# Kernel tuning notes

Hardware: AMD Instinct MI355X
Metric: run time of the kernel (lower is better)

## Reference

```python
import jax, jax.numpy as jnp
import numpy as np

NUM_EMBEDDINGS = 8192
EMBEDDING_DIM = 512
COMMITMENT_COST = 0.25


def setup_inputs() -> dict:
    key = jax.random.key(0)
    k1, k2 = jax.random.split(key)
    x = jax.random.normal(k1, (32768, EMBEDDING_DIM), dtype=jnp.float32)
    embeddings = jax.random.normal(k2, (NUM_EMBEDDINGS, EMBEDDING_DIM), dtype=jnp.float32) * 0.1
    return {"x": x, "embeddings": embeddings}


def reference(x, embeddings):
    # Flatten to (N, D)
    orig_shape = x.shape
    flat_x = x.reshape(-1, EMBEDDING_DIM)
    n = flat_x.shape[0]

    x_sq = jnp.sum(flat_x * flat_x, axis=1, keepdims=True)
    e_sq = jnp.sum(embeddings * embeddings, axis=1)
    dist = x_sq + e_sq - 2.0 * jnp.matmul(flat_x, embeddings.T)
    encoding_indices = jnp.argmin(dist, axis=1)  # (N,)

    # Codebook lookup (equivalent to one_hot @ embeddings)
    quantized = embeddings[encoding_indices].reshape(orig_shape)

    # Straight-through estimator
    quantized_st = x + jax.lax.stop_gradient(quantized - x)

    # Commitment loss (quantized detached)
    commitment_loss = COMMITMENT_COST * jnp.mean(
        (x - jax.lax.stop_gradient(quantized)) ** 2
    )

    # Perplexity from mean one-hot encodings (= normalized counts)
    counts = jnp.zeros((NUM_EMBEDDINGS,), dtype=jnp.float32).at[encoding_indices].add(1.0)
    avg_probs = counts / n
    perplexity = jnp.exp(-jnp.sum(avg_probs * jnp.log(avg_probs + 1e-10)))

    return quantized_st, commitment_loss, perplexity, encoding_indices
```

## Files before the change

### kernel.cpp

```cpp
#include <hip/hip_runtime.h>
#include <math.h>

#define N_ROWS 32768
#define K_CODES 8192
#define DIM 512
#define Q_OFF ((size_t)N_ROWS * DIM)

#define NSPLIT 2
#define KSPL (K_CODES / NSPLIT)
#define NPOOL (NSPLIT * 2)
#define MARGIN_V 0.025f

typedef _Float16 half8 __attribute__((ext_vector_type(8)));
typedef float f32x4 __attribute__((ext_vector_type(4)));

#define GLOAD_LDS(src, dst)                                                        \
  __builtin_amdgcn_global_load_lds(                                                \
      (const __attribute__((address_space(1))) void*)(src),                        \
      (__attribute__((address_space(3))) void*)(dst), 16, 0, 0)

__global__ __launch_bounds__(256) void vq_pack_f16(const float4* __restrict__ src,
                                                   half8* __restrict__ dst, int n8) {
    int i = blockIdx.x * 256 + threadIdx.x;
    if (i >= n8) return;
    float4 a = src[i * 2], b = src[i * 2 + 1];
    float v[8] = {a.x, a.y, a.z, a.w, b.x, b.y, b.z, b.w};
    half8 h;
#pragma unroll
    for (int k = 0; k < 8; ++k) h[k] = (_Float16)v[k];
    dst[i] = h;
}

__global__ __launch_bounds__(256) void vq_esq_init(const float* __restrict__ emb,
                                                   float* __restrict__ esqh,
                                                   int* __restrict__ counts) {
    int gid = blockIdx.x * 256 + threadIdx.x;
    if (gid < K_CODES) counts[gid] = 0;
    int code = gid >> 6;
    int lane = gid & 63;
    const float4* p = reinterpret_cast<const float4*>(emb + (size_t)code * DIM);
    float s = 0.f;
#pragma unroll
    for (int k = 0; k < 2; ++k) {
        float4 v = p[lane + 64 * k];
        s += v.x * v.x + v.y * v.y + v.z * v.z + v.w * v.w;
    }
#pragma unroll
    for (int off = 32; off > 0; off >>= 1) s += __shfl_down(s, off);
    if (lane == 0) esqh[code] = 0.5f * s;
}

__device__ __forceinline__ half8 fragq(const _Float16* t, int row, int kg) {
    return *reinterpret_cast<const half8*>(t + row * 32 + ((kg ^ ((row >> 2) & 3)) << 3));
}

__device__ __forceinline__ half8 frag16(const _Float16* t, int row, int kg) {
    return *reinterpret_cast<const half8*>(t + row * 32 + ((kg ^ (row & 3)) << 3));
}

__global__ __launch_bounds__(256, 2) void vq_argmin_f16q(
        const _Float16* __restrict__ xh, const _Float16* __restrict__ eh,
        const float* __restrict__ esqh,
        float* __restrict__ v1o, float* __restrict__ v2o,
        unsigned int* __restrict__ io) {
    __shared__ __align__(16) _Float16 sbuf[4][8192];

    const int tid = threadIdx.x;
    const int lane = tid & 63;
    const int wid = tid >> 6;
    const int wr = wid >> 1, wc = wid & 1;
    const int lr = lane & 15, kg = lane >> 4;
    const int row0 = blockIdx.x * 128;
    const int csplit0 = blockIdx.y * KSPL;

    int off[2], dstA[2], dstB[2];
#pragma unroll
    for (int c = 0; c < 2; ++c) {
        int r = wid * 32 + c * 16 + (lane >> 2);
        int sx = (lane & 3) ^ ((r >> 2) & 3);
        off[c] = r * DIM + sx * 8;
        dstA[c] = (wid * 32 + c * 16) * 32;
        dstB[c] = 4096 + dstA[c];
    }

    auto stage = [&](int b, int s) {
        int cc = s >> 4, ks = s & 15;
        const _Float16* a0 = xh + (size_t)row0 * DIM + ks * 32;
        const _Float16* b0 = eh + (size_t)(csplit0 + cc * 128) * DIM + ks * 32;
        _Float16* base = &sbuf[b][0];
#pragma unroll
        for (int c = 0; c < 2; ++c) {
            GLOAD_LDS(a0 + off[c], base + dstA[c]);
            GLOAD_LDS(b0 + off[c], base + dstB[c]);
        }
    };

    auto compute = [&](int bq, f32x4 (&acc)[4][4]) {
        const _Float16* A = &sbuf[bq][0];
        const _Float16* B = &sbuf[bq][4096];
        half8 a[4], b[4];
#pragma unroll
        for (int i = 0; i < 4; ++i) a[i] = fragq(A, wr * 64 + i * 16 + lr, kg);
#pragma unroll
        for (int j = 0; j < 4; ++j) b[j] = fragq(B, wc * 64 + j * 16 + lr, kg);
#pragma unroll
        for (int j = 0; j < 4; ++j)
#pragma unroll
            for (int i = 0; i < 4; ++i)
                acc[i][j] = __builtin_amdgcn_mfma_f32_16x16x32_f16(a[i], b[j], acc[i][j], 0, 0, 0);
    };

    float rv1[16], rv2[16];
    unsigned int ridx[16];
#pragma unroll
    for (int t = 0; t < 16; ++t) { rv1[t] = INFINITY; rv2[t] = INFINITY; ridx[t] = 0; }

    auto fold = [&](int cc, f32x4 (&acc)[4][4]) {
#pragma unroll
        for (int j = 0; j < 4; ++j) {
            int cg = csplit0 + cc * 128 + wc * 64 + j * 16 + lr;
            float eqv = esqh[cg];
#pragma unroll
            for (int i = 0; i < 4; ++i) {
#pragma unroll
                for (int r = 0; r < 4; ++r) {
                    float v = eqv - acc[i][j][r];
                    int t = i * 4 + r;
                    if (v < rv1[t]) {
                        rv2[t] = rv1[t]; ridx[t] = (ridx[t] << 16) | (unsigned int)cg; rv1[t] = v;
                    } else if (v < rv2[t]) {
                        rv2[t] = v; ridx[t] = (ridx[t] & 0xFFFFu) | ((unsigned int)cg << 16);
                    }
                }
            }
        }
    };

    const int NCC = KSPL / 128;
    stage(0, 0);
    stage(1, 1);

    for (int cc = 0; cc < NCC - 1; ++cc) {
        f32x4 acc[4][4];
#pragma unroll
        for (int i = 0; i < 4; ++i)
#pragma unroll
            for (int j = 0; j < 4; ++j) acc[i][j] = (f32x4)(0.f);
#pragma unroll
        for (int ks = 0; ks < 16; ++ks) {
            asm volatile("s_waitcnt vmcnt(4)" ::: "memory");
            __builtin_amdgcn_s_barrier();
            stage((ks + 2) & 3, cc * 16 + ks + 2);
            compute(ks & 3, acc);
        }
        fold(cc, acc);
    }
    {
        const int cc = NCC - 1;
        f32x4 acc[4][4];
#pragma unroll
        for (int i = 0; i < 4; ++i)
#pragma unroll
            for (int j = 0; j < 4; ++j) acc[i][j] = (f32x4)(0.f);
#pragma unroll
        for (int ks = 0; ks < 16; ++ks) {
            if (ks == 15) asm volatile("s_waitcnt vmcnt(0)" ::: "memory");
            else          asm volatile("s_waitcnt vmcnt(4)" ::: "memory");
            __builtin_amdgcn_s_barrier();
            if (ks < 14) stage((ks + 2) & 3, cc * 16 + ks + 2);
            compute(ks & 3, acc);
        }
        fold(cc, acc);
    }

#pragma unroll
    for (int m = 1; m <= 8; m <<= 1) {
#pragma unroll
        for (int t = 0; t < 16; ++t) {
            float bv1 = __shfl_xor(rv1[t], m);
            float bv2 = __shfl_xor(rv2[t], m);
            unsigned int ox = (unsigned int)__shfl_xor((int)ridx[t], m);
            unsigned int ai1 = ridx[t] & 0xFFFFu, ai2 = ridx[t] >> 16;
            unsigned int bi1 = ox & 0xFFFFu, bi2 = ox >> 16;
            float av1 = rv1[t], av2 = rv2[t];
            bool bf = (bv1 < av1) || (bv1 == av1 && bi1 < ai1);
            float n1v = bf ? bv1 : av1; unsigned int n1i = bf ? bi1 : ai1;
            float w1v = bf ? av1 : bv1; unsigned int w1i = bf ? ai1 : bi1;
            bool cf = (bv2 < av2) || (bv2 == av2 && bi2 < ai2);
            float c2v = cf ? bv2 : av2; unsigned int c2i = cf ? bi2 : ai2;
            bool df = (c2v < w1v) || (c2v == w1v && c2i < w1i);
            float n2v = df ? c2v : w1v; unsigned int n2i = df ? c2i : w1i;
            rv1[t] = n1v; rv2[t] = n2v; ridx[t] = n1i | (n2i << 16);
        }
    }

    if (lr == 0) {
#pragma unroll
        for (int t = 0; t < 16; ++t) {
            int rl = wr * 64 + (t >> 2) * 16 + kg * 4 + (t & 3);
            size_t o = (size_t)(blockIdx.y * 2 + wc) * N_ROWS + row0 + rl;
            v1o[o] = rv1[t]; v2o[o] = rv2[t]; io[o] = ridx[t];
        }
    }
}

__global__ __launch_bounds__(256, 2) void vq_argmin_fb(
        const float* __restrict__ xf, const float* __restrict__ ef,
        const float* __restrict__ esqh,
        float* __restrict__ v1o, float* __restrict__ v2o,
        unsigned int* __restrict__ io) {
    __shared__ __align__(16) _Float16 sbuf[2][12288];

    const int tid = threadIdx.x;
    const int lane = tid & 63;
    const int wid = tid >> 6;
    const int wr = wid >> 1, wc = wid & 1;
    const int lr = lane & 15, kg = lane >> 4;
    const int row0 = blockIdx.x * 128;
    const int csplit0 = blockIdx.y * KSPL;

    auto stage = [&](int b, int s) {
        int cc = s >> 4, ks = s & 15;
        {
            const int r = tid >> 1;
            const int k0 = (tid & 1) * 16;
            const float4* xp = reinterpret_cast<const float4*>(
                xf + (size_t)(row0 + r) * DIM + ks * 32 + k0);
            float4 f0 = xp[0], f1 = xp[1], f2 = xp[2], f3 = xp[3];
            float v[16] = {f0.x, f0.y, f0.z, f0.w, f1.x, f1.y, f1.z, f1.w,
                           f2.x, f2.y, f2.z, f2.w, f3.x, f3.y, f3.z, f3.w};
            half8 h0, h1;
#pragma unroll
            for (int k = 0; k < 8; ++k) { h0[k] = (_Float16)v[k]; h1[k] = (_Float16)v[8 + k]; }
            int s0 = (k0 >> 3) ^ (r & 3);
            int s1 = ((k0 >> 3) + 1) ^ (r & 3);
            _Float16* Ah = &sbuf[b][0];
            *reinterpret_cast<half8*>(Ah + r * 32 + s0 * 8) = h0;
            *reinterpret_cast<half8*>(Ah + r * 32 + s1 * 8) = h1;
        }
        {
            const int r = tid;
            const float4* ep = reinterpret_cast<const float4*>(
                ef + (size_t)(csplit0 + cc * 256 + r) * DIM + ks * 32);
            _Float16* Be = &sbuf[b][4096];
#pragma unroll
            for (int q = 0; q < 4; ++q) {
                float4 g0 = ep[q * 2], g1 = ep[q * 2 + 1];
                half8 h;
                h[0] = (_Float16)g0.x; h[1] = (_Float16)g0.y;
                h[2] = (_Float16)g0.z; h[3] = (_Float16)g0.w;
                h[4] = (_Float16)g1.x; h[5] = (_Float16)g1.y;
                h[6] = (_Float16)g1.z; h[7] = (_Float16)g1.w;
                *reinterpret_cast<half8*>(Be + r * 32 + ((q ^ (r & 3)) << 3)) = h;
            }
        }
    };

    float rv1[16], rv2[16];
    unsigned int ridx[16];
#pragma unroll
    for (int t = 0; t < 16; ++t) { rv1[t] = INFINITY; rv2[t] = INFINITY; ridx[t] = 0; }

    f32x4 acc[4][8];
    const int NS = (KSPL / 256) * 16;
    int cur = 0;
    stage(0, 0);
    __syncthreads();
    for (int s = 0; s < NS; ++s) {
        if ((s & 15) == 0) {
#pragma unroll
            for (int i = 0; i < 4; ++i)
#pragma unroll
                for (int j = 0; j < 8; ++j) acc[i][j] = (f32x4)(0.f);
        }
        const _Float16* Ah = &sbuf[cur][0];
        const _Float16* Be = &sbuf[cur][4096];
        half8 a[4];
#pragma unroll
        for (int i = 0; i < 4; ++i) a[i] = frag16(Ah, wr * 64 + i * 16 + lr, kg);
#pragma unroll
        for (int j = 0; j < 8; ++j) {
            half8 b = frag16(Be, wc * 128 + j * 16 + lr, kg);
#pragma unroll
            for (int i = 0; i < 4; ++i)
                acc[i][j] = __builtin_amdgcn_mfma_f32_16x16x32_f16(a[i], b, acc[i][j], 0, 0, 0);
        }
        if (s + 1 < NS) stage(cur ^ 1, s + 1);
        if ((s & 15) == 15) {
            int cc = s >> 4;
#pragma unroll
            for (int j = 0; j < 8; ++j) {
                int cg = csplit0 + cc * 256 + wc * 128 + j * 16 + lr;
                float eqv = esqh[cg];
#pragma unroll
                for (int i = 0; i < 4; ++i) {
#pragma unroll
                    for (int r = 0; r < 4; ++r) {
                        float v = eqv - acc[i][j][r];
                        int t = i * 4 + r;
                        if (v < rv1[t]) {
                            rv2[t] = rv1[t]; ridx[t] = (ridx[t] << 16) | (unsigned int)cg; rv1[t] = v;
                        } else if (v < rv2[t]) {
                            rv2[t] = v; ridx[t] = (ridx[t] & 0xFFFFu) | ((unsigned int)cg << 16);
                        }
                    }
                }
            }
        }
        __syncthreads();
        cur ^= 1;
    }

#pragma unroll
    for (int m = 1; m <= 8; m <<= 1) {
#pragma unroll
        for (int t = 0; t < 16; ++t) {
            float bv1 = __shfl_xor(rv1[t], m);
            float bv2 = __shfl_xor(rv2[t], m);
            unsigned int ox = (unsigned int)__shfl_xor((int)ridx[t], m);
            unsigned int ai1 = ridx[t] & 0xFFFFu, ai2 = ridx[t] >> 16;
            unsigned int bi1 = ox & 0xFFFFu, bi2 = ox >> 16;
            float av1 = rv1[t], av2 = rv2[t];
            bool bf = (bv1 < av1) || (bv1 == av1 && bi1 < ai1);
            float n1v = bf ? bv1 : av1; unsigned int n1i = bf ? bi1 : ai1;
            float w1v = bf ? av1 : bv1; unsigned int w1i = bf ? ai1 : bi1;
            bool cf = (bv2 < av2) || (bv2 == av2 && bi2 < ai2);
            float c2v = cf ? bv2 : av2; unsigned int c2i = cf ? bi2 : ai2;
            bool df = (c2v < w1v) || (c2v == w1v && c2i < w1i);
            float n2v = df ? c2v : w1v; unsigned int n2i = df ? c2i : w1i;
            rv1[t] = n1v; rv2[t] = n2v; ridx[t] = n1i | (n2i << 16);
        }
    }
    if (lr == 0) {
#pragma unroll
        for (int t = 0; t < 16; ++t) {
            int rl = wr * 64 + (t >> 2) * 16 + kg * 4 + (t & 3);
            size_t o = (size_t)(blockIdx.y * 2 + wc) * N_ROWS + row0 + rl;
            v1o[o] = rv1[t]; v2o[o] = rv2[t]; io[o] = ridx[t];
        }
    }
}

__global__ __launch_bounds__(64) void vq_gather(const float* __restrict__ x,
                                                const float* __restrict__ emb,
                                                const float* __restrict__ v1,
                                                const float* __restrict__ v2,
                                                const unsigned int* __restrict__ io,
                                                float* __restrict__ out,
                                                int* __restrict__ counts,
                                                float* __restrict__ lossp) {
    const int row = blockIdx.x;
    const int lane = threadIdx.x;

    float V1 = INFINITY, V2 = INFINITY;
    unsigned int I1 = 0xFFFFu, I2 = 0xFFFFu;
#pragma unroll
    for (int p = 0; p < NPOOL; ++p) {
        size_t o = (size_t)p * N_ROWS + row;
        float bv1 = v1[o], bv2 = v2[o];
        unsigned int ox = io[o];
        unsigned int bi1 = ox & 0xFFFFu, bi2 = ox >> 16;
        bool bf = (bv1 < V1) || (bv1 == V1 && bi1 < I1);
        float n1v = bf ? bv1 : V1; unsigned int n1i = bf ? bi1 : I1;
        float w1v = bf ? V1 : bv1; unsigned int w1i = bf ? I1 : bi1;
        bool cf = (bv2 < V2) || (bv2 == V2 && bi2 < I2);
        float c2v = cf ? bv2 : V2; unsigned int c2i = cf ? bi2 : I2;
        bool df = (c2v < w1v) || (c2v == w1v && c2i < w1i);
        V1 = n1v; I1 = n1i;
        V2 = df ? c2v : w1v; I2 = df ? c2i : w1i;
    }

    int c = (int)I1;
    if (V2 - V1 < MARGIN_V) {
        unsigned int cand[8];
#pragma unroll
        for (int p = 0; p < NPOOL; ++p) {
            unsigned int ox = io[(size_t)p * N_ROWS + row];
            cand[2 * p] = ox & 0xFFFFu;
            cand[2 * p + 1] = ox >> 16;
        }
        double xd[8];
#pragma unroll
        for (int kk = 0; kk < 8; ++kk)
            xd[kk] = (double)x[(size_t)row * DIM + lane + 64 * kk];
        double best = 1e300;
        unsigned int bi = 0xFFFFFFFFu;
#pragma unroll
        for (int t = 0; t < 8; ++t) {
            const float* e1 = emb + (size_t)cand[t] * DIM;
            double d = 0.0;
#pragma unroll
            for (int kk = 0; kk < 8; ++kk) {
                double df = xd[kk] - (double)e1[lane + 64 * kk];
                d = fma(df, df, d);
            }
#pragma unroll
            for (int m = 1; m <= 32; m <<= 1) d += __shfl_xor(d, m);
            if (d < best || (d == best && cand[t] < bi)) { best = d; bi = cand[t]; }
        }
        c = (int)bi;
    }

    const float4* xr4 = reinterpret_cast<const float4*>(x + (size_t)row * DIM);
    const float4* er4 = reinterpret_cast<const float4*>(emb + (size_t)c * DIM);
    float4* qo = reinterpret_cast<float4*>(out + (size_t)row * DIM);
    float lsum = 0.f;
#pragma unroll
    for (int k = 0; k < 2; ++k) {
        int idx = lane + 64 * k;
        float4 e = er4[idx];
        float4 xv = xr4[idx];
        qo[idx] = e;
        float dx = xv.x - e.x, dy = xv.y - e.y, dz = xv.z - e.z, dw = xv.w - e.w;
        lsum += dx * dx + dy * dy + dz * dz + dw * dw;
    }
#pragma unroll
    for (int off = 32; off > 0; off >>= 1) lsum += __shfl_down(lsum, off);
    if (lane == 0) {
        lossp[row] = lsum;
        atomicAdd(&counts[c], 1);
        out[Q_OFF + 2 + row] = (float)c;
    }
}

__global__ __launch_bounds__(256) void vq_finalize(const float* __restrict__ lossp,
                                                   const int* __restrict__ counts,
                                                   float* __restrict__ out) {
    __shared__ double sred[8];
    const int tid = threadIdx.x;
    const int lane = tid & 63, wv = tid >> 6;
    double ls = 0.0, hs = 0.0;
    for (int r = tid; r < N_ROWS; r += 256) ls += (double)lossp[r];
    for (int cidx = tid; cidx < K_CODES; cidx += 256) {
        double p = (double)counts[cidx] * (1.0 / (double)N_ROWS);
        hs += p * log(p + 1e-10);
    }
#pragma unroll
    for (int off = 32; off > 0; off >>= 1) {
        ls += __shfl_down(ls, off);
        hs += __shfl_down(hs, off);
    }
    if (lane == 0) { sred[wv] = ls; sred[4 + wv] = hs; }
    __syncthreads();
    if (tid == 0) {
        double L = sred[0] + sred[1] + sred[2] + sred[3];
        double H = sred[4] + sred[5] + sred[6] + sred[7];
        out[Q_OFF]     = (float)(0.25 * L / (double)Q_OFF);
        out[Q_OFF + 1] = (float)exp(-H);
    }
}

extern "C" void kernel_launch(void* const* d_in, const int* in_sizes, int n_in,
                              void* d_out, int out_size, void* d_ws, size_t ws_size,
                              hipStream_t stream) {
    const float* x   = (const float*)d_in[0];
    const float* emb = (const float*)d_in[1];
    float* out = (float*)d_out;

    unsigned int* w = (unsigned int*)d_ws;
    float* esqh         = (float*)(w);
    int*   counts       = (int*)(w + 8192);
    float* lossp        = (float*)(w + 16384);
    float* v1           = (float*)(w + 49152);
    float* v2           = (float*)(w + 180224);
    unsigned int* io    = (unsigned int*)(w + 311296);
    _Float16* x_h       = (_Float16*)(w + 442368);
    _Float16* e_h       = (_Float16*)(w + 8830976);
    const size_t need   = (size_t)10928128 * 4;

    const bool pk = ws_size >= need;

    vq_esq_init<<<(K_CODES * 64) / 256, 256, 0, stream>>>(emb, esqh, counts);
    if (pk) {
        vq_pack_f16<<<(N_ROWS * DIM / 8) / 256, 256, 0, stream>>>(
            (const float4*)x, (half8*)x_h, N_ROWS * DIM / 8);
        vq_pack_f16<<<(K_CODES * DIM / 8) / 256, 256, 0, stream>>>(
            (const float4*)emb, (half8*)e_h, K_CODES * DIM / 8);
    }

    dim3 grid(N_ROWS / 128, NSPLIT);
    if (pk)
        vq_argmin_f16q<<<grid, 256, 0, stream>>>(x_h, e_h, esqh, v1, v2, io);
    else
        vq_argmin_fb<<<grid, 256, 0, stream>>>(x, emb, esqh, v1, v2, io);

    vq_gather<<<N_ROWS, 64, 0, stream>>>(x, emb, v1, v2, io, out, counts, lossp);
    vq_finalize<<<1, 256, 0, stream>>>(lossp, counts, out);
}
```

Baseline: 457.0 us.

## Enlarge argmin GEMM tile to 256x256 with 512 threads and double buffering

Result: slower. 625.0 us (+36.8%).

```diff
diff --git a/kernel.cpp b/kernel.cpp
--- a/kernel.cpp
+++ b/kernel.cpp
@@ -50,28 +50,26 @@
     if (lane == 0) esqh[code] = 0.5f * s;
 }
 
-__device__ __forceinline__ half8 fragq(const _Float16* t, int row, int kg) {
-    return *reinterpret_cast<const half8*>(t + row * 32 + ((kg ^ ((row >> 2) & 3)) << 3));
-}
-
 __device__ __forceinline__ half8 frag16(const _Float16* t, int row, int kg) {
     return *reinterpret_cast<const half8*>(t + row * 32 + ((kg ^ (row & 3)) << 3));
 }
 
-__global__ __launch_bounds__(256, 2) void vq_argmin_f16q(
+__global__ __launch_bounds__(512, 2) void vq_argmin_f16w(
         const _Float16* __restrict__ xh, const _Float16* __restrict__ eh,
         const float* __restrict__ esqh,
         float* __restrict__ v1o, float* __restrict__ v2o,
         unsigned int* __restrict__ io) {
-    __shared__ __align__(16) _Float16 sbuf[4][8192];
+    __shared__ __align__(16) _Float16 sbuf[2][16384];
 
     const int tid = threadIdx.x;
     const int lane = tid & 63;
     const int wid = tid >> 6;
-    const int wr = wid >> 1, wc = wid & 1;
+    const int wr = wid >> 1;
+    const int wc = wid & 1;
     const int lr = lane & 15, kg = lane >> 4;
-    const int row0 = blockIdx.x * 128;
+    const int row0 = blockIdx.x * 256;
     const int csplit0 = blockIdx.y * KSPL;
+    const int NCC = KSPL / 256;
 
     int off[2], dstA[2], dstB[2];
 #pragma unroll
@@ -80,13 +78,12 @@
         int sx = (lane & 3) ^ ((r >> 2) & 3);
         off[c] = r * DIM + sx * 8;
         dstA[c] = (wid * 32 + c * 16) * 32;
-        dstB[c] = 4096 + dstA[c];
-    }
-
-    auto stage = [&](int b, int s) {
-        int cc = s >> 4, ks = s & 15;
+        dstB[c] = 8192 + dstA[c];
+    }
+
+    auto stage = [&](int b, int cc, int ks) {
         const _Float16* a0 = xh + (size_t)row0 * DIM + ks * 32;
-        const _Float16* b0 = eh + (size_t)(csplit0 + cc * 128) * DIM + ks * 32;
+        const _Float16* b0 = eh + (size_t)(csplit0 + cc * 256) * DIM + ks * 32;
         _Float16* base = &sbuf[b][0];
 #pragma unroll
         for (int c = 0; c < 2; ++c) {
@@ -95,16 +92,20 @@
         }
     };
 
-    auto compute = [&](int bq, f32x4 (&acc)[4][4]) {
-        const _Float16* A = &sbuf[bq][0];
-        const _Float16* B = &sbuf[bq][4096];
-        half8 a[4], b[4];
-#pragma unroll
-        for (int i = 0; i < 4; ++i) a[i] = fragq(A, wr * 64 + i * 16 + lr, kg);
-#pragma unroll
-        for (int j = 0; j < 4; ++j) b[j] = fragq(B, wc * 64 + j * 16 + lr, kg);
-#pragma unroll
-        for (int j = 0; j < 4; ++j)
+    const int swz = (kg ^ ((lr >> 2) & 3)) << 3;
+    const int aB = (wr * 64 + lr) * 32 + swz;
+    const int bB = 8192 + (wc * 128 + lr) * 32 + swz;
+
+    auto compute = [&](const _Float16* base, f32x4 (&acc)[4][8]) {
+        half8 a[4], b[8];
+#pragma unroll
+        for (int i = 0; i < 4; ++i)
+            a[i] = *reinterpret_cast<const half8*>(base + aB + i * 512);
+#pragma unroll
+        for (int j = 0; j < 8; ++j)
+            b[j] = *reinterpret_cast<const half8*>(base + bB + j * 512);
+#pragma unroll
+        for (int j = 0; j < 8; ++j)
 #pragma unroll
             for (int i = 0; i < 4; ++i)
                 acc[i][j] = __builtin_amdgcn_mfma_f32_16x16x32_f16(a[i], b[j], acc[i][j], 0, 0, 0);
@@ -115,10 +116,10 @@
 #pragma unroll
     for (int t = 0; t < 16; ++t) { rv1[t] = INFINITY; rv2[t] = INFINITY; ridx[t] = 0; }
 
-    auto fold = [&](int cc, f32x4 (&acc)[4][4]) {
-#pragma unroll
-        for (int j = 0; j < 4; ++j) {
-            int cg = csplit0 + cc * 128 + wc * 64 + j * 16 + lr;
+    auto fold = [&](int cc, f32x4 (&acc)[4][8]) {
+#pragma unroll
+        for (int j = 0; j < 8; ++j) {
+            int cg = csplit0 + cc * 256 + wc * 128 + j * 16 + lr;
             float eqv = esqh[cg];
 #pragma unroll
             for (int i = 0; i < 4; ++i) {
@@ -136,39 +137,21 @@
         }
     };
 
-    const int NCC = KSPL / 128;
-    stage(0, 0);
-    stage(1, 1);
-
-    for (int cc = 0; cc < NCC - 1; ++cc) {
-        f32x4 acc[4][4];
+    stage(0, 0, 0);
+    __syncthreads();
+
+    for (int cc = 0; cc < NCC; ++cc) {
+        f32x4 acc[4][8];
 #pragma unroll
         for (int i = 0; i < 4; ++i)
 #pragma unroll
-            for (int j = 0; j < 4; ++j) acc[i][j] = (f32x4)(0.f);
+            for (int j = 0; j < 8; ++j) acc[i][j] = (f32x4)(0.f);
 #pragma unroll
         for (int ks = 0; ks < 16; ++ks) {
-            asm volatile("s_waitcnt vmcnt(4)" ::: "memory");
-            __builtin_amdgcn_s_barrier();
-            stage((ks + 2) & 3, cc * 16 + ks + 2);
-            compute(ks & 3, acc);
-        }
-        fold(cc, acc);
-    }
-    {
-        const int cc = NCC - 1;
-        f32x4 acc[4][4];
-#pragma unroll
-        for (int i = 0; i < 4; ++i)
-#pragma unroll
-            for (int j = 0; j < 4; ++j) acc[i][j] = (f32x4)(0.f);
-#pragma unroll
-        for (int ks = 0; ks < 16; ++ks) {
-            if (ks == 15) asm volatile("s_waitcnt vmcnt(0)" ::: "memory");
-            else          asm volatile("s_waitcnt vmcnt(4)" ::: "memory");
-            __builtin_amdgcn_s_barrier();
-            if (ks < 14) stage((ks + 2) & 3, cc * 16 + ks + 2);
-            compute(ks & 3, acc);
+            if (!(cc == NCC - 1 && ks == 15))
+                stage((ks + 1) & 1, cc + (ks == 15 ? 1 : 0), (ks + 1) & 15);
+            compute(&sbuf[ks & 1][0], acc);
+            __syncthreads();
         }
         fold(cc, acc);
     }
@@ -478,11 +461,13 @@
             (const float4*)emb, (half8*)e_h, K_CODES * DIM / 8);
     }
 
-    dim3 grid(N_ROWS / 128, NSPLIT);
-    if (pk)
-        vq_argmin_f16q<<<grid, 256, 0, stream>>>(x_h, e_h, esqh, v1, v2, io);
-    else
+    if (pk) {
+        dim3 grid(N_ROWS / 256, NSPLIT);
+        vq_argmin_f16w<<<grid, 512, 0, stream>>>(x_h, e_h, esqh, v1, v2, io);
+    } else {
+        dim3 grid(N_ROWS / 128, NSPLIT);
         vq_argmin_fb<<<grid, 256, 0, stream>>>(x, emb, esqh, v1, v2, io);
+    }
 
     vq_gather<<<N_ROWS, 64, 0, stream>>>(x, emb, v1, v2, io, out, counts, lossp);
     vq_finalize<<<1, 256, 0, stream>>>(lossp, counts, out);
```
